# Kernel tuning notes

Hardware: AMD Instinct MI355X
Metric: run time of the kernel (lower is better)

Reference implementation:

```python
import jax, jax.numpy as jnp
import numpy as np

B, S, D, H = 4, 2048, 1024, 16
HD = D // H  # head dim = 64


def setup_inputs() -> dict:
    key = jax.random.key(0)
    k1, k2, k3 = jax.random.split(key, 3)
    scale = 1.0 / np.sqrt(D).astype(np.float32)
    x = jax.random.normal(k1, (B, S, D), dtype=jnp.float32)
    # q/k slices of nn.MultiheadAttention's in_proj (v and out_proj never
    # influence the returned values since x_t is discarded by forward)
    wq = jax.random.normal(k2, (D, D), dtype=jnp.float32) * scale
    wk = jax.random.normal(k3, (D, D), dtype=jnp.float32) * scale
    bq = jnp.zeros((D,), dtype=jnp.float32)
    bk = jnp.zeros((D,), dtype=jnp.float32)
    # 8 contiguous scale blocks of 256 tokens; last boundary == S
    scales_idx = (jnp.arange(1, 9, dtype=jnp.int64) * (S // 8))
    return {"x": x, "wq": wq, "wk": wk, "bq": bq, "bk": bk,
            "scales_idx": scales_idx}


def reference(x, wq, wk, bq, bk, scales_idx):
    b, s, d = x.shape
    # project q, k and split heads: [B, H, S, HD]
    q = (x @ wq.T + bq).reshape(b, s, H, HD).transpose(0, 2, 1, 3)
    k = (x @ wk.T + bk).reshape(b, s, H, HD).transpose(0, 2, 1, 3)
    inv_sqrt_hd = jnp.asarray(1.0 / np.sqrt(HD), dtype=x.dtype)
    scores = jnp.einsum('bhqd,bhkd->bhqk', q, k) * inv_sqrt_hd  # [B,H,S,S]
    # block-diagonal mask: token i belongs to the block whose right boundary
    # is the first scales_idx entry strictly greater than i
    pos = jnp.arange(s)
    seg = jnp.searchsorted(scales_idx, pos, side='right')  # [S]
    allowed = seg[:, None] == seg[None, :]                  # [S,S] bool
    scores = jnp.where(allowed[None, None], scores, -jnp.inf)
    w = jax.nn.softmax(scores, axis=-1)  # every row has >=1 allowed entry
    weights_attn = jnp.mean(w, axis=1)   # average over heads -> [B,S,S]
    return (x, weights_attn)
```

## Files before the change

kernel.cpp:

```cpp
#include <hip/hip_runtime.h>
#include <hip/hip_bf16.h>
#include <math.h>

#define BB 4
#define SS 2048
#define DD 1024
#define HH 16
#define HD 64
#define MM (BB*SS)
#define NN (2*DD)
#define BK 64
#define NKT 16

typedef __attribute__((ext_vector_type(8))) short short8;
typedef __attribute__((ext_vector_type(4))) float f32x4;
typedef unsigned short ushort_t;

__device__ __forceinline__ void gload16(const void* g, void* l) {
    __builtin_amdgcn_global_load_lds((const __attribute__((address_space(1))) unsigned int*)g,
                                     (__attribute__((address_space(3))) unsigned int*)l,
                                     16, 0, 0);
}

__global__ __launch_bounds__(256)
void copy_cast(const float* __restrict__ x, float* __restrict__ out_x,
               __hip_bfloat16* __restrict__ xb, int n8)
{
    int i = blockIdx.x * 256 + threadIdx.x;
    if (i >= n8) return;
    const float4* s = (const float4*)x + (size_t)i * 2;
    float4 a = s[0], b = s[1];
    float4* o = (float4*)out_x + (size_t)i * 2;
    o[0] = a; o[1] = b;
    __hip_bfloat16 tmp[8];
    tmp[0] = __float2bfloat16(a.x); tmp[1] = __float2bfloat16(a.y);
    tmp[2] = __float2bfloat16(a.z); tmp[3] = __float2bfloat16(a.w);
    tmp[4] = __float2bfloat16(b.x); tmp[5] = __float2bfloat16(b.y);
    tmp[6] = __float2bfloat16(b.z); tmp[7] = __float2bfloat16(b.w);
    *(float4*)&xb[(size_t)i * 8] = *(float4*)tmp;
}

__global__ __launch_bounds__(256)
void cast_w(const float* __restrict__ wq, const float* __restrict__ wk,
            __hip_bfloat16* __restrict__ wb)
{
    const int half = (DD * DD) / 8;
    int i = blockIdx.x * 256 + threadIdx.x;
    if (i >= 2 * half) return;
    const float* src = (i < half) ? wq : wk;
    int j = (i < half) ? i : i - half;
    const float4* s = (const float4*)src + (size_t)j * 2;
    float4 a = s[0], b = s[1];
    __hip_bfloat16 tmp[8];
    tmp[0] = __float2bfloat16(a.x); tmp[1] = __float2bfloat16(a.y);
    tmp[2] = __float2bfloat16(a.z); tmp[3] = __float2bfloat16(a.w);
    tmp[4] = __float2bfloat16(b.x); tmp[5] = __float2bfloat16(b.y);
    tmp[6] = __float2bfloat16(b.z); tmp[7] = __float2bfloat16(b.w);
    *(float4*)&wb[(size_t)i * 8] = *(float4*)tmp;
}

__device__ __forceinline__ void stage_A(const ushort_t* __restrict__ xb, ushort_t* Ab,
                                        int m0, int kt, int mh, int wv, int lane)
{
    #pragma unroll
    for (int it = 0; it < 2; ++it) {
        int rl0 = it * 64 + wv * 8;
        int r0 = (rl0 & 63) + ((rl0 >> 6) << 7) + mh * 64;
        int r  = r0 + (lane >> 3);
        int gch = (lane & 7) ^ (r & 7);
        gload16(xb + (size_t)(m0 + r) * DD + kt + gch * 8, Ab + r0 * 64);
    }
}

__device__ __forceinline__ void stage_Bt(const ushort_t* __restrict__ wb, ushort_t* Bb,
                                         int n0, int kt, int nh, int wv, int lane)
{
    #pragma unroll
    for (int it = 0; it < 2; ++it) {
        int rl0 = it * 64 + wv * 8;
        int r0 = (rl0 & 31) + ((rl0 >> 5) << 6) + nh * 32;
        int r  = r0 + (lane >> 3);
        int gch = (lane & 7) ^ (r & 7);
        gload16(wb + (size_t)(n0 + r) * DD + kt + gch * 8, Bb + r0 * 64);
    }
}

__global__ __launch_bounds__(512, 2)
void proj_mfma(const ushort_t* __restrict__ xb, const ushort_t* __restrict__ wb,
               const float* __restrict__ bq, const float* __restrict__ bk,
               __hip_bfloat16* __restrict__ Qb, __hip_bfloat16* __restrict__ Kb)
{
    __shared__ __align__(16) ushort_t As[2][256 * BK];
    __shared__ __align__(16) ushort_t Bs[2][256 * BK];

    const int t = threadIdx.x;
    const int wv = t >> 6, lane = t & 63, quad = lane >> 4, l15 = lane & 15;
    const int wr = wv >> 2, wc = wv & 3;
    const int m0 = blockIdx.x * 256, n0 = blockIdx.y * 256;

    f32x4 acc[8][4];
    #pragma unroll
    for (int mt = 0; mt < 8; ++mt)
        #pragma unroll
        for (int nt = 0; nt < 4; ++nt) acc[mt][nt] = (f32x4){0.f, 0.f, 0.f, 0.f};

    stage_Bt(wb, Bs[0], n0, 0, 0, wv, lane);
    stage_A (xb, As[0], m0, 0, 0, wv, lane);
    stage_A (xb, As[0], m0, 0, 1, wv, lane);
    stage_Bt(wb, Bs[0], n0, 0, 1, wv, lane);
    stage_Bt(wb, Bs[1], n0, BK, 0, wv, lane);
    stage_A (xb, As[1], m0, BK, 0, wv, lane);
    asm volatile("s_waitcnt vmcnt(4)" ::: "memory");
    __builtin_amdgcn_s_barrier();

    #pragma unroll 1
    for (int tt = 0; tt < NKT; ++tt) {
        ushort_t* Ac = As[tt & 1];
        ushort_t* Bc = Bs[tt & 1];
        ushort_t* An = As[(tt & 1) ^ 1];
        ushort_t* Bn = Bs[(tt & 1) ^ 1];
        short8 a[8][2], b[2][2];

        #pragma unroll
        for (int mt = 0; mt < 4; ++mt)
            #pragma unroll
            for (int ks = 0; ks < 2; ++ks) {
                int r = wr * 128 + mt * 16 + l15;
                int sl = r * 8 + ((ks * 4 + quad) ^ (r & 7));
                a[mt][ks] = *(const short8*)&Ac[sl * 8];
            }
        #pragma unroll
        for (int nt = 0; nt < 2; ++nt)
            #pragma unroll
            for (int ks = 0; ks < 2; ++ks) {
                int r = wc * 64 + nt * 16 + l15;
                int sl = r * 8 + ((ks * 4 + quad) ^ (r & 7));
                b[nt][ks] = *(const short8*)&Bc[sl * 8];
            }
        if (tt + 1 < NKT) stage_A(xb, An, m0, (tt + 1) * BK, 1, wv, lane);
        __builtin_amdgcn_s_barrier();
        asm volatile("s_waitcnt lgkmcnt(0)" ::: "memory");
        __builtin_amdgcn_sched_barrier(0);
        __builtin_amdgcn_s_setprio(1);
        #pragma unroll
        for (int mt = 0; mt < 4; ++mt)
            #pragma unroll
            for (int nt = 0; nt < 2; ++nt)
                #pragma unroll
                for (int ks = 0; ks < 2; ++ks)
                    acc[mt][nt] = __builtin_amdgcn_mfma_f32_16x16x32_bf16(
                        a[mt][ks], b[nt][ks], acc[mt][nt], 0, 0, 0);
        __builtin_amdgcn_s_setprio(0);
        __builtin_amdgcn_sched_barrier(0);
        __builtin_amdgcn_s_barrier();

        #pragma unroll
        for (int mt = 0; mt < 4; ++mt)
            #pragma unroll
            for (int ks = 0; ks < 2; ++ks) {
                int r = wr * 128 + 64 + mt * 16 + l15;
                int sl = r * 8 + ((ks * 4 + quad) ^ (r & 7));
                a[4 + mt][ks] = *(const short8*)&Ac[sl * 8];
            }
        if (tt + 1 < NKT) stage_Bt(wb, Bn, n0, (tt + 1) * BK, 1, wv, lane);
        __builtin_amdgcn_s_barrier();
        asm volatile("s_waitcnt lgkmcnt(0)" ::: "memory");
        __builtin_amdgcn_sched_barrier(0);
        __builtin_amdgcn_s_setprio(1);
        #pragma unroll
        for (int mt = 0; mt < 4; ++mt)
            #pragma unroll
            for (int nt = 0; nt < 2; ++nt)
                #pragma unroll
                for (int ks = 0; ks < 2; ++ks)
                    acc[4 + mt][nt] = __builtin_amdgcn_mfma_f32_16x16x32_bf16(
                        a[4 + mt][ks], b[nt][ks], acc[4 + mt][nt], 0, 0, 0);
        __builtin_amdgcn_s_setprio(0);
        __builtin_amdgcn_sched_barrier(0);
        __builtin_amdgcn_s_barrier();

        #pragma unroll
        for (int nt = 0; nt < 2; ++nt)
            #pragma unroll
            for (int ks = 0; ks < 2; ++ks) {
                int r = wc * 64 + 32 + nt * 16 + l15;
                int sl = r * 8 + ((ks * 4 + quad) ^ (r & 7));
                b[nt][ks] = *(const short8*)&Bc[sl * 8];
            }
        if (tt + 2 < NKT) stage_Bt(wb, Bc, n0, (tt + 2) * BK, 0, wv, lane);
        __builtin_amdgcn_s_barrier();
        asm volatile("s_waitcnt lgkmcnt(0)" ::: "memory");
        __builtin_amdgcn_sched_barrier(0);
        __builtin_amdgcn_s_setprio(1);
        #pragma unroll
        for (int mt = 0; mt < 4; ++mt)
            #pragma unroll
            for (int nt = 0; nt < 2; ++nt)
                #pragma unroll
                for (int ks = 0; ks < 2; ++ks)
                    acc[mt][2 + nt] = __builtin_amdgcn_mfma_f32_16x16x32_bf16(
                        a[mt][ks], b[nt][ks], acc[mt][2 + nt], 0, 0, 0);
        __builtin_amdgcn_s_setprio(0);
        __builtin_amdgcn_sched_barrier(0);
        __builtin_amdgcn_s_barrier();

        if (tt + 2 < NKT) stage_A(xb, Ac, m0, (tt + 2) * BK, 0, wv, lane);
        __builtin_amdgcn_s_barrier();
        asm volatile("s_waitcnt lgkmcnt(0)" ::: "memory");
        __builtin_amdgcn_sched_barrier(0);
        __builtin_amdgcn_s_setprio(1);
        #pragma unroll
        for (int mt = 0; mt < 4; ++mt)
            #pragma unroll
            for (int nt = 0; nt < 2; ++nt)
                #pragma unroll
                for (int ks = 0; ks < 2; ++ks)
                    acc[4 + mt][2 + nt] = __builtin_amdgcn_mfma_f32_16x16x32_bf16(
                        a[4 + mt][ks], b[nt][ks], acc[4 + mt][2 + nt], 0, 0, 0);
        __builtin_amdgcn_s_setprio(0);
        __builtin_amdgcn_sched_barrier(0);
        if (tt < NKT - 2)       asm volatile("s_waitcnt vmcnt(4)" ::: "memory");
        else if (tt == NKT - 2) asm volatile("s_waitcnt vmcnt(0)" ::: "memory");
        __builtin_amdgcn_s_barrier();
    }

    const bool isQ = (n0 < DD);
    const float* bias = isQ ? bq : bk;
    __hip_bfloat16* outp = isQ ? Qb : Kb;
    const int nc0 = (isQ ? n0 : n0 - DD) + wc * 64;
    #pragma unroll
    for (int nt = 0; nt < 4; ++nt) {
        const int nc = nc0 + nt * 16 + l15;
        const float bv = bias[nc];
        #pragma unroll
        for (int mt = 0; mt < 8; ++mt)
            #pragma unroll
            for (int reg = 0; reg < 4; ++reg) {
                int m = m0 + wr * 128 + mt * 16 + quad * 4 + reg;
                outp[(size_t)m * DD + nc] = __float2bfloat16(acc[mt][nt][reg] + bv);
            }
    }
}

__global__ __launch_bounds__(256, 1)
void attn_block(const ushort_t* __restrict__ Qb, const ushort_t* __restrict__ Kb,
                const int* __restrict__ scales, float* __restrict__ outw)
{
    __shared__ __align__(16) char smem[73728];
    ushort_t* KsB = (ushort_t*)smem;
    ushort_t* QsB = (ushort_t*)(smem + 65536);
    float (*comb)[256] = (float(*)[256])smem;

    const int bid = blockIdx.x;
    const int rt  = bid >> 5;
    const int blk = bid & 7, bb = (bid >> 3) & 3;
    const int start = blk ? scales[blk - 1] : 0;

    const int t = threadIdx.x;
    const int wv = t >> 6, lane = t & 63, quad = lane >> 4, l15 = lane & 15;
    const int rg = wv & 1, hg = wv >> 1;

    f32x4 accm[16];
    #pragma unroll
    for (int nt = 0; nt < 16; ++nt) accm[nt] = (f32x4){0.f, 0.f, 0.f, 0.f};

    const int qrow0 = start + rt * 32;

    for (int i = 0; i < 8; ++i) {
        __syncthreads();
        #pragma unroll
        for (int half = 0; half < 2; ++half) {
            const int h = half * 8 + i;
            ushort_t* Kl = KsB + half * (256 * 64);
            ushort_t* Ql = QsB + half * (32 * 64);
            #pragma unroll
            for (int round = 0; round < 8; ++round) {
                int c = round * 256 + t;
                int row = c >> 3, ch = c & 7;
                int gch = ch ^ (row & 7);
                gload16(Kb + (size_t)(bb * SS + start + row) * DD + h * HD + gch * 8,
                        Kl + ((size_t)round * 256 + wv * 64) * 8);
            }
            {
                int row = t >> 3, ch = t & 7;
                int gch = ch ^ (row & 7);
                gload16(Qb + (size_t)(bb * SS + qrow0 + row) * DD + h * HD + gch * 8,
                        Ql + ((size_t)wv * 64) * 8);
            }
        }
        __syncthreads();

        const ushort_t* Ks = KsB + hg * (256 * 64);
        const ushort_t* Qs = QsB + hg * (32 * 64);

        short8 af[2];
        #pragma unroll
        for (int ks = 0; ks < 2; ++ks) {
            int qr = rg * 16 + l15;
            int sl = qr * 8 + ((ks * 4 + quad) ^ (qr & 7));
            af[ks] = *(const short8*)&Qs[sl * 8];
        }
        f32x4 sc[16];
        #pragma unroll
        for (int nt = 0; nt < 16; ++nt) {
            sc[nt] = (f32x4){0.f, 0.f, 0.f, 0.f};
            #pragma unroll
            for (int ks = 0; ks < 2; ++ks) {
                int kr = nt * 16 + l15;
                int sl = kr * 8 + ((ks * 4 + quad) ^ (kr & 7));
                short8 bf = *(const short8*)&Ks[sl * 8];
                sc[nt] = __builtin_amdgcn_mfma_f32_16x16x32_bf16(af[ks], bf, sc[nt], 0, 0, 0);
            }
        }
        float rs[4] = {0.f, 0.f, 0.f, 0.f};
        #pragma unroll
        for (int nt = 0; nt < 16; ++nt) {
            #pragma unroll
            for (int r = 0; r < 4; ++r) {
                float p = __expf(sc[nt][r] * 0.125f);
                sc[nt][r] = p;
                rs[r] += p;
            }
        }
        #pragma unroll
        for (int r = 0; r < 4; ++r) {
            #pragma unroll
            for (int off = 1; off < 16; off <<= 1) rs[r] += __shfl_xor(rs[r], off, 64);
            rs[r] = 1.0f / rs[r];
        }
        #pragma unroll
        for (int nt = 0; nt < 16; ++nt)
            #pragma unroll
            for (int r = 0; r < 4; ++r) accm[nt][r] += sc[nt][r] * rs[r];
    }

    __syncthreads();
    if (hg == 0) {
        #pragma unroll
        for (int nt = 0; nt < 16; ++nt)
            #pragma unroll
            for (int r = 0; r < 4; ++r)
                comb[rg * 16 + quad * 4 + r][nt * 16 + l15] = accm[nt][r];
    }
    __syncthreads();
    if (hg == 1) {
        #pragma unroll
        for (int nt = 0; nt < 16; ++nt)
            #pragma unroll
            for (int r = 0; r < 4; ++r)
                comb[rg * 16 + quad * 4 + r][nt * 16 + l15] += accm[nt][r];
    }
    __syncthreads();

    const float s16 = 1.0f / (float)HH;
    const size_t orow0 = (size_t)bb * SS + qrow0;
    #pragma unroll
    for (int it = 0; it < 64; ++it) {
        int flat = it * 256 + t;
        int row = flat >> 9;
        int col = (flat & 511) * 4;
        float4 v = make_float4(0.f, 0.f, 0.f, 0.f);
        unsigned lc = (unsigned)(col - start);
        if (lc < 256u) {
            const float* c = &comb[row][lc];
            v = make_float4(c[0] * s16, c[1] * s16, c[2] * s16, c[3] * s16);
        }
        *(float4*)&outw[(orow0 + row) * SS + col] = v;
    }
}

extern "C" void kernel_launch(void* const* d_in, const int* in_sizes, int n_in,
                              void* d_out, int out_size, void* d_ws, size_t ws_size,
                              hipStream_t stream)
{
    const float* x  = (const float*)d_in[0];
    const float* wq = (const float*)d_in[1];
    const float* wk = (const float*)d_in[2];
    const float* bq = (const float*)d_in[3];
    const float* bk = (const float*)d_in[4];
    const int* scales = (const int*)d_in[5];

    float* out_x = (float*)d_out;
    float* out_w = out_x + (size_t)BB * SS * DD;

    char* w = (char*)d_ws;
    __hip_bfloat16* xb = (__hip_bfloat16*)(w);
    __hip_bfloat16* wb = (__hip_bfloat16*)(w + 16777216);
    __hip_bfloat16* Qb = (__hip_bfloat16*)(w + 20971520);
    __hip_bfloat16* Kb = (__hip_bfloat16*)(w + 37748736);

    copy_cast<<<4096, 256, 0, stream>>>(x, out_x, xb, (MM * DD) / 8);
    cast_w<<<1024, 256, 0, stream>>>(wq, wk, wb);

    dim3 pgrid(MM / 256, NN / 256);
    proj_mfma<<<pgrid, 512, 0, stream>>>((const ushort_t*)xb, (const ushort_t*)wb,
                                         bq, bk, Qb, Kb);

    attn_block<<<256, 256, 0, stream>>>((const ushort_t*)Qb, (const ushort_t*)Kb,
                                        scales, out_w);
}
```

Before: 208.0 us.

## Pipeline GEMM LDS reads, double-buffer attention K/Q staging, use nontemporal stores

```diff
diff --git a/kernel.cpp b/kernel.cpp
--- a/kernel.cpp
+++ b/kernel.cpp
@@ -28,10 +28,11 @@
 {
     int i = blockIdx.x * 256 + threadIdx.x;
     if (i >= n8) return;
-    const float4* s = (const float4*)x + (size_t)i * 2;
-    float4 a = s[0], b = s[1];
-    float4* o = (float4*)out_x + (size_t)i * 2;
-    o[0] = a; o[1] = b;
+    const f32x4* s = (const f32x4*)x + (size_t)i * 2;
+    f32x4 a = s[0], b = s[1];
+    f32x4* o = (f32x4*)out_x + (size_t)i * 2;
+    __builtin_nontemporal_store(a, o);
+    __builtin_nontemporal_store(b, o + 1);
     __hip_bfloat16 tmp[8];
     tmp[0] = __float2bfloat16(a.x); tmp[1] = __float2bfloat16(a.y);
     tmp[2] = __float2bfloat16(a.z); tmp[3] = __float2bfloat16(a.w);
@@ -104,14 +105,51 @@
         #pragma unroll
         for (int nt = 0; nt < 4; ++nt) acc[mt][nt] = (f32x4){0.f, 0.f, 0.f, 0.f};
 
+    short8 a0[4][2], a1[4][2], b0[2][2], b1[2][2];
+
+#define RD_A(buf, mh, dst)                                            \
+    _Pragma("unroll")                                                 \
+    for (int mt_ = 0; mt_ < 4; ++mt_) {                               \
+        _Pragma("unroll")                                             \
+        for (int ks_ = 0; ks_ < 2; ++ks_) {                           \
+            int r_ = wr * 128 + (mh) * 64 + mt_ * 16 + l15;           \
+            int sl_ = r_ * 8 + ((ks_ * 4 + quad) ^ (r_ & 7));         \
+            dst[mt_][ks_] = *(const short8*)&(buf)[sl_ * 8];          \
+        }                                                             \
+    }
+#define RD_B(buf, nh, dst)                                            \
+    _Pragma("unroll")                                                 \
+    for (int nt_ = 0; nt_ < 2; ++nt_) {                               \
+        _Pragma("unroll")                                             \
+        for (int ks_ = 0; ks_ < 2; ++ks_) {                           \
+            int r_ = wc * 64 + (nh) * 32 + nt_ * 16 + l15;            \
+            int sl_ = r_ * 8 + ((ks_ * 4 + quad) ^ (r_ & 7));         \
+            dst[nt_][ks_] = *(const short8*)&(buf)[sl_ * 8];          \
+        }                                                             \
+    }
+#define MFMA_Q(A_, B_, mo, no)                                        \
+    _Pragma("unroll")                                                 \
+    for (int mt_ = 0; mt_ < 4; ++mt_)                                 \
+        _Pragma("unroll")                                             \
+        for (int nt_ = 0; nt_ < 2; ++nt_)                             \
+            _Pragma("unroll")                                         \
+            for (int ks_ = 0; ks_ < 2; ++ks_)                         \
+                acc[(mo) + mt_][(no) + nt_] =                         \
+                    __builtin_amdgcn_mfma_f32_16x16x32_bf16(          \
+                        A_[mt_][ks_], B_[nt_][ks_],                   \
+                        acc[(mo) + mt_][(no) + nt_], 0, 0, 0);
+
     stage_Bt(wb, Bs[0], n0, 0, 0, wv, lane);
     stage_A (xb, As[0], m0, 0, 0, wv, lane);
+    stage_Bt(wb, Bs[0], n0, 0, 1, wv, lane);
     stage_A (xb, As[0], m0, 0, 1, wv, lane);
-    stage_Bt(wb, Bs[0], n0, 0, 1, wv, lane);
-    stage_Bt(wb, Bs[1], n0, BK, 0, wv, lane);
-    stage_A (xb, As[1], m0, BK, 0, wv, lane);
+    stage_Bt(wb, Bs[1], n0, BK, 1, wv, lane);
+    stage_A (xb, As[1], m0, BK, 1, wv, lane);
     asm volatile("s_waitcnt vmcnt(4)" ::: "memory");
     __builtin_amdgcn_s_barrier();
+    RD_A(As[0], 0, a0);
+    RD_B(Bs[0], 0, b0);
+    __builtin_amdgcn_sched_barrier(0);
 
     #pragma unroll 1
     for (int tt = 0; tt < NKT; ++tt) {
@@ -119,108 +157,53 @@
         ushort_t* Bc = Bs[tt & 1];
         ushort_t* An = As[(tt & 1) ^ 1];
         ushort_t* Bn = Bs[(tt & 1) ^ 1];
-        short8 a[8][2], b[2][2];
-
-        #pragma unroll
-        for (int mt = 0; mt < 4; ++mt)
-            #pragma unroll
-            for (int ks = 0; ks < 2; ++ks) {
-                int r = wr * 128 + mt * 16 + l15;
-                int sl = r * 8 + ((ks * 4 + quad) ^ (r & 7));
-                a[mt][ks] = *(const short8*)&Ac[sl * 8];
-            }
-        #pragma unroll
-        for (int nt = 0; nt < 2; ++nt)
-            #pragma unroll
-            for (int ks = 0; ks < 2; ++ks) {
-                int r = wc * 64 + nt * 16 + l15;
-                int sl = r * 8 + ((ks * 4 + quad) ^ (r & 7));
-                b[nt][ks] = *(const short8*)&Bc[sl * 8];
-            }
-        if (tt + 1 < NKT) stage_A(xb, An, m0, (tt + 1) * BK, 1, wv, lane);
-        __builtin_amdgcn_s_barrier();
+
+        if (tt + 1 < NKT) stage_Bt(wb, Bn, n0, (tt + 1) * BK, 0, wv, lane);
+        RD_B(Bc, 1, b1);
+        __builtin_amdgcn_sched_barrier(0);
+        asm volatile("s_waitcnt lgkmcnt(4)" ::: "memory");
+        __builtin_amdgcn_sched_barrier(0);
+        __builtin_amdgcn_s_setprio(1);
+        MFMA_Q(a0, b0, 0, 0);
+        __builtin_amdgcn_s_setprio(0);
+        __builtin_amdgcn_sched_barrier(0);
+        __builtin_amdgcn_s_barrier();
+
+        if (tt + 1 < NKT) stage_A(xb, An, m0, (tt + 1) * BK, 0, wv, lane);
+        RD_A(Ac, 1, a1);
+        __builtin_amdgcn_sched_barrier(0);
+        asm volatile("s_waitcnt lgkmcnt(8)" ::: "memory");
+        __builtin_amdgcn_sched_barrier(0);
+        __builtin_amdgcn_s_setprio(1);
+        MFMA_Q(a0, b1, 0, 2);
+        __builtin_amdgcn_s_setprio(0);
+        __builtin_amdgcn_sched_barrier(0);
+        __builtin_amdgcn_s_barrier();
+
         asm volatile("s_waitcnt lgkmcnt(0)" ::: "memory");
         __builtin_amdgcn_sched_barrier(0);
         __builtin_amdgcn_s_setprio(1);
-        #pragma unroll
-        for (int mt = 0; mt < 4; ++mt)
-            #pragma unroll
-            for (int nt = 0; nt < 2; ++nt)
-                #pragma unroll
-                for (int ks = 0; ks < 2; ++ks)
-                    acc[mt][nt] = __builtin_amdgcn_mfma_f32_16x16x32_bf16(
-                        a[mt][ks], b[nt][ks], acc[mt][nt], 0, 0, 0);
+        MFMA_Q(a1, b0, 4, 0);
         __builtin_amdgcn_s_setprio(0);
         __builtin_amdgcn_sched_barrier(0);
         __builtin_amdgcn_s_barrier();
 
-        #pragma unroll
-        for (int mt = 0; mt < 4; ++mt)
-            #pragma unroll
-            for (int ks = 0; ks < 2; ++ks) {
-                int r = wr * 128 + 64 + mt * 16 + l15;
-                int sl = r * 8 + ((ks * 4 + quad) ^ (r & 7));
-                a[4 + mt][ks] = *(const short8*)&Ac[sl * 8];
-            }
-        if (tt + 1 < NKT) stage_Bt(wb, Bn, n0, (tt + 1) * BK, 1, wv, lane);
-        __builtin_amdgcn_s_barrier();
-        asm volatile("s_waitcnt lgkmcnt(0)" ::: "memory");
-        __builtin_amdgcn_sched_barrier(0);
-        __builtin_amdgcn_s_setprio(1);
-        #pragma unroll
-        for (int mt = 0; mt < 4; ++mt)
-            #pragma unroll
-            for (int nt = 0; nt < 2; ++nt)
-                #pragma unroll
-                for (int ks = 0; ks < 2; ++ks)
-                    acc[4 + mt][nt] = __builtin_amdgcn_mfma_f32_16x16x32_bf16(
-                        a[4 + mt][ks], b[nt][ks], acc[4 + mt][nt], 0, 0, 0);
-        __builtin_amdgcn_s_setprio(0);
-        __builtin_amdgcn_sched_barrier(0);
-        __builtin_amdgcn_s_barrier();
-
-        #pragma unroll
-        for (int nt = 0; nt < 2; ++nt)
-            #pragma unroll
-            for (int ks = 0; ks < 2; ++ks) {
-                int r = wc * 64 + 32 + nt * 16 + l15;
-                int sl = r * 8 + ((ks * 4 + quad) ^ (r & 7));
-                b[nt][ks] = *(const short8*)&Bc[sl * 8];
-            }
-        if (tt + 2 < NKT) stage_Bt(wb, Bc, n0, (tt + 2) * BK, 0, wv, lane);
-        __builtin_amdgcn_s_barrier();
-        asm volatile("s_waitcnt lgkmcnt(0)" ::: "memory");
-        __builtin_amdgcn_sched_barrier(0);
-        __builtin_amdgcn_s_setprio(1);
-        #pragma unroll
-        for (int mt = 0; mt < 4; ++mt)
-            #pragma unroll
-            for (int nt = 0; nt < 2; ++nt)
-                #pragma unroll
-                for (int ks = 0; ks < 2; ++ks)
-                    acc[mt][2 + nt] = __builtin_amdgcn_mfma_f32_16x16x32_bf16(
-                        a[mt][ks], b[nt][ks], acc[mt][2 + nt], 0, 0, 0);
-        __builtin_amdgcn_s_setprio(0);
-        __builtin_amdgcn_sched_barrier(0);
-        __builtin_amdgcn_s_barrier();
-
-        if (tt + 2 < NKT) stage_A(xb, Ac, m0, (tt + 2) * BK, 0, wv, lane);
-        __builtin_amdgcn_s_barrier();
-        asm volatile("s_waitcnt lgkmcnt(0)" ::: "memory");
-        __builtin_amdgcn_sched_barrier(0);
-        __builtin_amdgcn_s_setprio(1);
-        #pragma unroll
-        for (int mt = 0; mt < 4; ++mt)
-            #pragma unroll
-            for (int nt = 0; nt < 2; ++nt)
-                #pragma unroll
-                for (int ks = 0; ks < 2; ++ks)
-                    acc[4 + mt][2 + nt] = __builtin_amdgcn_mfma_f32_16x16x32_bf16(
-                        a[4 + mt][ks], b[nt][ks], acc[4 + mt][2 + nt], 0, 0, 0);
-        __builtin_amdgcn_s_setprio(0);
-        __builtin_amdgcn_sched_barrier(0);
+        if (tt + 2 < NKT) {
+            stage_Bt(wb, Bc, n0, (tt + 2) * BK, 1, wv, lane);
+            stage_A (xb, Ac, m0, (tt + 2) * BK, 1, wv, lane);
+        }
         if (tt < NKT - 2)       asm volatile("s_waitcnt vmcnt(4)" ::: "memory");
         else if (tt == NKT - 2) asm volatile("s_waitcnt vmcnt(0)" ::: "memory");
+        __builtin_amdgcn_s_barrier();
+        if (tt + 1 < NKT) {
+            RD_A(An, 0, a0);
+            RD_B(Bn, 0, b0);
+        }
+        __builtin_amdgcn_sched_barrier(0);
+        __builtin_amdgcn_s_setprio(1);
+        MFMA_Q(a1, b1, 4, 2);
+        __builtin_amdgcn_s_setprio(0);
+        __builtin_amdgcn_sched_barrier(0);
         __builtin_amdgcn_s_barrier();
     }
 
@@ -240,15 +223,16 @@
                 outp[(size_t)m * DD + nc] = __float2bfloat16(acc[mt][nt][reg] + bv);
             }
     }
+#undef RD_A
+#undef RD_B
+#undef MFMA_Q
 }
 
 __global__ __launch_bounds__(256, 1)
 void attn_block(const ushort_t* __restrict__ Qb, const ushort_t* __restrict__ Kb,
                 const int* __restrict__ scales, float* __restrict__ outw)
 {
-    __shared__ __align__(16) char smem[73728];
-    ushort_t* KsB = (ushort_t*)smem;
-    ushort_t* QsB = (ushort_t*)(smem + 65536);
+    __shared__ __align__(16) char smem[147456];
     float (*comb)[256] = (float(*)[256])smem;
 
     const int bid = blockIdx.x;
@@ -265,33 +249,44 @@
     for (int nt = 0; nt < 16; ++nt) accm[nt] = (f32x4){0.f, 0.f, 0.f, 0.f};
 
     const int qrow0 = start + rt * 32;
-
-    for (int i = 0; i < 8; ++i) {
-        __syncthreads();
+    const int brow  = bb * SS;
+
+    auto stageKQ = [&](int i, int buf) {
         #pragma unroll
         for (int half = 0; half < 2; ++half) {
             const int h = half * 8 + i;
-            ushort_t* Kl = KsB + half * (256 * 64);
-            ushort_t* Ql = QsB + half * (32 * 64);
+            ushort_t* Kl = (ushort_t*)(smem + (size_t)(buf * 2 + half) * 32768);
+            ushort_t* Ql = (ushort_t*)(smem + 131072 + (size_t)(buf * 2 + half) * 4096);
             #pragma unroll
             for (int round = 0; round < 8; ++round) {
                 int c = round * 256 + t;
                 int row = c >> 3, ch = c & 7;
                 int gch = ch ^ (row & 7);
-                gload16(Kb + (size_t)(bb * SS + start + row) * DD + h * HD + gch * 8,
+                gload16(Kb + (size_t)(brow + start + row) * DD + h * HD + gch * 8,
                         Kl + ((size_t)round * 256 + wv * 64) * 8);
             }
             {
                 int row = t >> 3, ch = t & 7;
                 int gch = ch ^ (row & 7);
-                gload16(Qb + (size_t)(bb * SS + qrow0 + row) * DD + h * HD + gch * 8,
+                gload16(Qb + (size_t)(brow + qrow0 + row) * DD + h * HD + gch * 8,
                         Ql + ((size_t)wv * 64) * 8);
             }
         }
-        __syncthreads();
-
-        const ushort_t* Ks = KsB + hg * (256 * 64);
-        const ushort_t* Qs = QsB + hg * (32 * 64);
+    };
+
+    stageKQ(0, 0);
+
+    for (int i = 0; i < 8; ++i) {
+        if (i < 7) {
+            stageKQ(i + 1, (i + 1) & 1);
+            asm volatile("s_waitcnt vmcnt(18)" ::: "memory");
+        } else {
+            asm volatile("s_waitcnt vmcnt(0)" ::: "memory");
+        }
+        __builtin_amdgcn_s_barrier();
+
+        const ushort_t* Ks = (const ushort_t*)(smem + (size_t)((i & 1) * 2 + hg) * 32768);
+        const ushort_t* Qs = (const ushort_t*)(smem + 131072 + (size_t)((i & 1) * 2 + hg) * 4096);
 
         short8 af[2];
         #pragma unroll
@@ -332,6 +327,8 @@
         for (int nt = 0; nt < 16; ++nt)
             #pragma unroll
             for (int r = 0; r < 4; ++r) accm[nt][r] += sc[nt][r] * rs[r];
+
+        __builtin_amdgcn_s_barrier();
     }
 
     __syncthreads();
@@ -359,13 +356,13 @@
         int flat = it * 256 + t;
         int row = flat >> 9;
         int col = (flat & 511) * 4;
-        float4 v = make_float4(0.f, 0.f, 0.f, 0.f);
+        f32x4 v = (f32x4){0.f, 0.f, 0.f, 0.f};
         unsigned lc = (unsigned)(col - start);
         if (lc < 256u) {
             const float* c = &comb[row][lc];
-            v = make_float4(c[0] * s16, c[1] * s16, c[2] * s16, c[3] * s16);
-        }
-        *(float4*)&outw[(orow0 + row) * SS + col] = v;
+            v = (f32x4){c[0] * s16, c[1] * s16, c[2] * s16, c[3] * s16};
+        }
+        __builtin_nontemporal_store(v, (f32x4*)&outw[(orow0 + row) * SS + col]);
     }
 }
 
```

After: 236.9 us. +13.9%, slower.
